# Optimization experiments

Measured on AMD Instinct MI355X. Metric: run time of the kernel, lower is better.

## Reference

```python
import jax, jax.numpy as jnp
import numpy as np

D = 2048
NUM_HEADS = 16
HEAD_DIM = D // NUM_HEADS
B, T = 4, 2048
NEG = -1e9


def setup_inputs() -> dict:
    key = jax.random.key(0)
    ks = jax.random.split(key, 6)
    X = jax.random.normal(ks[0], (B, T, D), dtype=jnp.float32)
    # additive causal mask, broadcast over batch and heads
    causal = jnp.tril(jnp.ones((T, T), dtype=jnp.float32))
    mask = jnp.where(causal == 1, 0.0, NEG)[None, None, :, :]
    scale = np.sqrt(2.0 / D).astype(np.float32)
    wq_w = jax.random.normal(ks[1], (D, D), dtype=jnp.float32) * scale
    wk_w = jax.random.normal(ks[2], (D, D), dtype=jnp.float32) * scale
    wv_w = jax.random.normal(ks[3], (D, D), dtype=jnp.float32) * scale
    wo_w = jax.random.normal(ks[4], (D, D), dtype=jnp.float32) * scale
    zeros = jnp.zeros((D,), dtype=jnp.float32)
    return {
        "X": X, "mask": mask,
        "wq_w": wq_w, "wq_b": zeros,
        "wk_w": wk_w, "wk_b": zeros,
        "wv_w": wv_w, "wv_b": zeros,
        "wo_w": wo_w, "wo_b": zeros,
    }


def reference(X, mask, wq_w, wq_b, wk_w, wk_b, wv_w, wv_b, wo_w, wo_b):
    b, t, d = X.shape
    # project and split heads: [b, h, t, hd]
    def proj(w, bias):
        return (X @ w + bias).reshape(b, t, NUM_HEADS, HEAD_DIM).transpose(0, 2, 1, 3)
    Q = proj(wq_w, wq_b)
    K = proj(wk_w, wk_b)
    V = proj(wv_w, wv_b)
    scores = jnp.einsum("bhqd,bhkd->bhqk", Q, K) / np.sqrt(HEAD_DIM).astype(X.dtype)
    scores = scores + mask
    A = jax.nn.softmax(scores, axis=-1)
    ctx = jnp.einsum("bhqk,bhkd->bhqd", A, V)  # [b, h, t, hd]
    ctx = ctx.transpose(0, 2, 1, 3).reshape(b, t, d)
    return ctx @ wo_w + wo_b
```

## Files before the change

### kernel.cpp

```cpp
#include <hip/hip_runtime.h>
#include <stdint.h>

#define DMODEL 2048
#define NH 16
#define HD 128
#define BATCH 4
#define SEQ 2048
#define MTOT (BATCH * SEQ)
#define LOG2E 1.44269504088896340736f

typedef __bf16 bf16x8 __attribute__((ext_vector_type(8)));
typedef float floatx4 __attribute__((ext_vector_type(4)));

__device__ __forceinline__ uint16_t f2b(float f) {
    union { float f; uint32_t i; } v; v.f = f;
    uint32_t r = v.i + 0x7fffu + ((v.i >> 16) & 1u);
    return (uint16_t)(r >> 16);
}

#define GLD16(gp, lp)                                                          \
    __builtin_amdgcn_global_load_lds(                                          \
        (__attribute__((address_space(1))) unsigned int*)(gp),                 \
        (__attribute__((address_space(3))) unsigned int*)(lp), 16, 0, 0)

#define WAITVMC(N) asm volatile("s_waitcnt vmcnt(" #N ")" ::: "memory")
#define WAITLGKM0                                                              \
    do {                                                                       \
        asm volatile("s_waitcnt lgkmcnt(0)" ::: "memory");                     \
        __builtin_amdgcn_sched_barrier(0);                                     \
    } while (0)

__global__ __launch_bounds__(256) void cvt_bf16(const float* __restrict__ in,
                                                uint16_t* __restrict__ out, int n) {
    const int i = (blockIdx.x * 256 + threadIdx.x) * 8;
    if (i >= n) return;
    const float4 a = *(const float4*)(in + i);
    const float4 b = *(const float4*)(in + i + 4);
    uint16_t v[8] __attribute__((aligned(16))) = {
        f2b(a.x), f2b(a.y), f2b(a.z), f2b(a.w),
        f2b(b.x), f2b(b.y), f2b(b.z), f2b(b.w)};
    *(uint4*)(out + i) = *(const uint4*)v;
}

__global__ __launch_bounds__(256) void tr_wf(const float* __restrict__ in,
                                             uint16_t* __restrict__ out) {
    __shared__ float t[64 * 69];
    const int tid = threadIdx.x;
    const int r0 = blockIdx.y * 64, c0 = blockIdx.x * 64;
    const int rr = tid >> 2, c16 = (tid & 3) << 4;
#pragma unroll
    for (int j = 0; j < 4; j++)
        *(float4*)&t[rr * 69 + c16 + j * 4] =
            *(const float4*)(in + (size_t)(r0 + rr) * DMODEL + c0 + c16 + j * 4);
    __syncthreads();
    const int oc = tid >> 2, r16 = (tid & 3) << 4;
    uint16_t v[16] __attribute__((aligned(16)));
#pragma unroll
    for (int j = 0; j < 16; j++) v[j] = f2b(t[(r16 + j) * 69 + oc]);
    uint16_t* o = out + (size_t)(c0 + oc) * DMODEL + r0 + r16;
    *(uint4*)o = *(const uint4*)v;
    *(uint4*)(o + 8) = *(const uint4*)(v + 8);
}

__global__ __launch_bounds__(512, 2) void gemm256(const uint16_t* __restrict__ A,
                                                  const uint16_t* __restrict__ Bt,
                                                  const float* __restrict__ bias,
                                                  void* __restrict__ Cout,
                                                  float scale, int mode, int tld) {
    __shared__ __attribute__((aligned(16))) uint16_t As[2][32 * 512];
    __shared__ __attribute__((aligned(16))) uint16_t Bs[2][32 * 512];

    const int tid = threadIdx.x, lane = tid & 63, w = tid >> 6;
    const int wr = w >> 2, wc = w & 3;
    const int col = lane & 15, quad = lane >> 4;

    const int nwg = gridDim.x, cpx = nwg >> 3;
    const int swz = ((int)blockIdx.x & 7) * cpx + ((int)blockIdx.x >> 3);
    const long m0 = (long)(swz >> 3) * 256;
    const long n0 = (long)(swz & 7) * 256;

    const uint16_t* Ab = A + (m0 + col) * (size_t)DMODEL + quad * 8;
    const uint16_t* Bb = Bt + (n0 + col) * (size_t)DMODEL + quad * 8;

#define STAGE256(bf, kt)                                                       \
    {                                                                          \
        const size_t kb = (size_t)(kt) * 64;                                   \
        _Pragma("unroll") for (int j = 0; j < 4; j++) {                        \
            const int blk = w * 4 + j;                                         \
            const size_t off =                                                 \
                kb + (size_t)(blk >> 1) * (16 * DMODEL) + (size_t)(blk & 1) * 32; \
            GLD16(Ab + off, &As[bf][blk * 512]);                               \
            GLD16(Bb + off, &Bs[bf][blk * 512]);                               \
        }                                                                      \
    }

    floatx4 acc[8][4];
#pragma unroll
    for (int m = 0; m < 8; m++)
#pragma unroll
        for (int n = 0; n < 4; n++) acc[m][n] = (floatx4){0.f, 0.f, 0.f, 0.f};

    const int NT = DMODEL / 64;
    STAGE256(0, 0);
    STAGE256(1, 1);

#pragma unroll 1
    for (int kt = 0; kt < NT; ++kt) {
        const int cur = kt & 1;
        if (kt == NT - 1) { WAITVMC(0); } else { WAITVMC(8); }
        __builtin_amdgcn_s_barrier();

        bf16x8 a0[8], b0[4];
#pragma unroll
        for (int m = 0; m < 8; m++)
            a0[m] = *(const bf16x8*)&As[cur][((wr * 8 + m) * 2 + 0) * 512 + lane * 8];
#pragma unroll
        for (int n = 0; n < 4; n++)
            b0[n] = *(const bf16x8*)&Bs[cur][((wc * 4 + n) * 2 + 0) * 512 + lane * 8];
        __builtin_amdgcn_s_setprio(1);
#pragma unroll
        for (int m = 0; m < 8; m++)
#pragma unroll
            for (int n = 0; n < 4; n++)
                acc[m][n] = __builtin_amdgcn_mfma_f32_16x16x32_bf16(a0[m], b0[n],
                                                                    acc[m][n], 0, 0, 0);
        __builtin_amdgcn_s_setprio(0);

        bf16x8 a1[8], b1[4];
#pragma unroll
        for (int m = 0; m < 8; m++)
            a1[m] = *(const bf16x8*)&As[cur][((wr * 8 + m) * 2 + 1) * 512 + lane * 8];
#pragma unroll
        for (int n = 0; n < 4; n++)
            b1[n] = *(const bf16x8*)&Bs[cur][((wc * 4 + n) * 2 + 1) * 512 + lane * 8];
        WAITLGKM0;
        __builtin_amdgcn_s_barrier();
        if (kt + 2 < NT) STAGE256(cur, kt + 2);
        __builtin_amdgcn_s_setprio(1);
#pragma unroll
        for (int m = 0; m < 8; m++)
#pragma unroll
            for (int n = 0; n < 4; n++)
                acc[m][n] = __builtin_amdgcn_mfma_f32_16x16x32_bf16(a1[m], b1[n],
                                                                    acc[m][n], 0, 0, 0);
        __builtin_amdgcn_s_setprio(0);
    }

    float bv[4];
#pragma unroll
    for (int n = 0; n < 4; n++) bv[n] = bias[n0 + wc * 64 + n * 16 + col];
#pragma unroll
    for (int m = 0; m < 8; m++) {
        const long row = m0 + wr * 128 + m * 16 + quad * 4;
#pragma unroll
        for (int n = 0; n < 4; n++) {
            const long cc = n0 + wc * 64 + n * 16 + col;
            if (mode == 2) {
                uint16_t tmp[4] __attribute__((aligned(8)));
#pragma unroll
                for (int r = 0; r < 4; r++)
                    tmp[r] = f2b((acc[m][n][r] + bv[n]) * scale);
                *(uint2*)&((uint16_t*)Cout)[(size_t)cc * tld + row] =
                    *(const uint2*)tmp;
            } else {
#pragma unroll
                for (int r = 0; r < 4; r++) {
                    const float v = (acc[m][n][r] + bv[n]) * scale;
                    const long idx = (row + r) * DMODEL + cc;
                    if (mode == 1) ((float*)Cout)[idx] = v;
                    else           ((uint16_t*)Cout)[idx] = f2b(v);
                }
            }
        }
    }
#undef STAGE256
}

__global__ __launch_bounds__(256, 2) void gemm(const uint16_t* __restrict__ A,
                                               const uint16_t* __restrict__ Bt,
                                               const float* __restrict__ bias,
                                               void* __restrict__ Cout,
                                               float scale, int mode, int tld) {
    __shared__ __attribute__((aligned(16))) uint16_t As[128 * 32];
    __shared__ __attribute__((aligned(16))) uint16_t Bs[128 * 32];
    const int tid = threadIdx.x, lane = tid & 63, w = tid >> 6;
    const int wr = w >> 1, wc = w & 1;
    const int col = lane & 15, quad = lane >> 4;
    const long m0 = (long)blockIdx.y * 128, n0 = (long)blockIdx.x * 128;

    floatx4 acc[4][4];
#pragma unroll
    for (int i = 0; i < 4; i++)
#pragma unroll
        for (int j = 0; j < 4; j++) acc[i][j] = (floatx4){0.f, 0.f, 0.f, 0.f};

    const int srow = tid >> 2, sc = (tid & 3) << 3;
    const uint16_t* Ag0 = A + (m0 + srow) * DMODEL + sc;
    const uint16_t* Bg0 = Bt + (n0 + srow) * DMODEL + sc;
    const long rstep = (long)64 * DMODEL;
    uint16_t* AsW = &As[w * 512];
    uint16_t* BsW = &Bs[w * 512];

    for (int kt = 0; kt < DMODEL; kt += 32) {
        GLD16(Ag0 + kt, AsW);
        GLD16(Ag0 + rstep + kt, AsW + 2048);
        GLD16(Bg0 + kt, BsW);
        GLD16(Bg0 + rstep + kt, BsW + 2048);
        __syncthreads();
        bf16x8 af[4], bfr[4];
#pragma unroll
        for (int i = 0; i < 4; i++)
            af[i] = *(const bf16x8*)&As[(wr * 64 + i * 16 + col) * 32 + quad * 8];
#pragma unroll
        for (int j = 0; j < 4; j++)
            bfr[j] = *(const bf16x8*)&Bs[(wc * 64 + j * 16 + col) * 32 + quad * 8];
#pragma unroll
        for (int i = 0; i < 4; i++)
#pragma unroll
            for (int j = 0; j < 4; j++)
                acc[i][j] = __builtin_amdgcn_mfma_f32_16x16x32_bf16(af[i], bfr[j],
                                                                    acc[i][j], 0, 0, 0);
        __syncthreads();
    }

    float bv[4];
#pragma unroll
    for (int j = 0; j < 4; j++) bv[j] = bias[n0 + wc * 64 + j * 16 + col];
#pragma unroll
    for (int i = 0; i < 4; i++) {
        const long row = m0 + wr * 64 + i * 16 + quad * 4;
#pragma unroll
        for (int j = 0; j < 4; j++) {
            const long cc = n0 + wc * 64 + j * 16 + col;
            if (mode == 2) {
                uint16_t tmp[4] __attribute__((aligned(8)));
#pragma unroll
                for (int r = 0; r < 4; r++)
                    tmp[r] = f2b((acc[i][j][r] + bv[j]) * scale);
                *(uint2*)&((uint16_t*)Cout)[(size_t)cc * tld + row] =
                    *(const uint2*)tmp;
            } else {
#pragma unroll
                for (int r = 0; r < 4; r++) {
                    const float v = (acc[i][j][r] + bv[j]) * scale;
                    const long idx = (row + r) * DMODEL + cc;
                    if (mode == 1) ((float*)Cout)[idx] = v;
                    else           ((uint16_t*)Cout)[idx] = f2b(v);
                }
            }
        }
    }
}

__global__ __launch_bounds__(256, 2) void flash(uint16_t* __restrict__ QO,
                                                const uint16_t* __restrict__ Kp,
                                                const uint16_t* __restrict__ Vt,
                                                int vld) {
    __shared__ __attribute__((aligned(16))) uint16_t Ks[16 * 512];
    __shared__ __attribute__((aligned(16))) uint16_t Vs[16 * 512];
    __shared__ __attribute__((aligned(16))) uint16_t Ps[4][32 * 88];

    const int tid = threadIdx.x, lane = tid & 63, w = tid >> 6;
    const int col = lane & 15, quad = lane >> 4;
    const int h = blockIdx.y & 15, b = blockIdx.y >> 4;
    const size_t brow = (size_t)b * SEQ;

    const uint16_t* kbase = Kp + brow * DMODEL + h * HD;
    const uint16_t* vtbase = Vt + (size_t)(h * HD) * vld + brow;
    const uint16_t* kg0 = kbase + (size_t)(w * 16 + col) * DMODEL + quad * 8;
    const uint16_t* vg0 = vtbase + (size_t)(w * 32 + col) * vld + quad * 8;

    for (int half = 0; half < 2; ++half) {
        const int qi = half ? (int)blockIdx.x : (15 - (int)blockIdx.x);
        const int q0 = qi * 128;
        uint16_t* qbase = QO + (brow + q0 + w * 32) * DMODEL + h * HD;

        bf16x8 qf[2][4];
#pragma unroll
        for (int i = 0; i < 2; i++)
#pragma unroll
            for (int kk = 0; kk < 4; kk++)
                qf[i][kk] = *(const bf16x8*)(qbase + (size_t)(i * 16 + col) * DMODEL +
                                             kk * 32 + quad * 8);

        floatx4 accO[2][8];
#pragma unroll
        for (int i = 0; i < 2; i++)
#pragma unroll
            for (int jd = 0; jd < 8; jd++) accO[i][jd] = (floatx4){0.f, 0.f, 0.f, 0.f};
        float mrun[2][4], lrun[2][4];
#pragma unroll
        for (int i = 0; i < 2; i++)
#pragma unroll
            for (int r = 0; r < 4; r++) { mrun[i][r] = -1e30f; lrun[i][r] = 0.f; }

        const int nkt = 2 * qi + 2;

        uint4 kv[4], vv4[4];
        {
#pragma unroll
            for (int p = 0; p < 4; p++)
                kv[p] = *(const uint4*)(kg0 + p * 32);
#pragma unroll
            for (int s = 0; s < 2; s++)
#pragma unroll
                for (int k2 = 0; k2 < 2; k2++)
                    vv4[s * 2 + k2] =
                        *(const uint4*)(vg0 + (size_t)s * 16 * vld + k2 * 32);
        }

        for (int ki = 0; ki < nkt; ki++) {
            const int key0 = ki * 64;
#pragma unroll
            for (int p = 0; p < 4; p++)
                *(uint4*)&Ks[(w * 4 + p) * 512 + lane * 8] = kv[p];
#pragma unroll
            for (int s = 0; s < 2; s++)
#pragma unroll
                for (int k2 = 0; k2 < 2; k2++)
                    *(uint4*)&Vs[((w * 2 + s) * 2 + k2) * 512 + lane * 8] =
                        vv4[s * 2 + k2];
            __syncthreads();

            if (ki + 1 < nkt) {
                const size_t koff = (size_t)(key0 + 64);
#pragma unroll
                for (int p = 0; p < 4; p++)
                    kv[p] = *(const uint4*)(kg0 + koff * DMODEL + p * 32);
#pragma unroll
                for (int s = 0; s < 2; s++)
#pragma unroll
                    for (int k2 = 0; k2 < 2; k2++)
                        vv4[s * 2 + k2] = *(const uint4*)(vg0 + (size_t)s * 16 * vld +
                                                          koff + k2 * 32);
            }

            floatx4 s[2][4];
            __builtin_amdgcn_s_setprio(1);
#pragma unroll
            for (int i = 0; i < 2; i++)
#pragma unroll
                for (int jk = 0; jk < 4; jk++) {
                    floatx4 a = (floatx4){0.f, 0.f, 0.f, 0.f};
#pragma unroll
                    for (int kk = 0; kk < 4; kk++) {
                        bf16x8 bb = *(const bf16x8*)&Ks[(jk * 4 + kk) * 512 + lane * 8];
                        a = __builtin_amdgcn_mfma_f32_16x16x32_bf16(qf[i][kk], bb, a, 0, 0, 0);
                    }
                    s[i][jk] = a;
                }
            __builtin_amdgcn_s_setprio(0);

            if (key0 + 63 > q0 + w * 32) {
#pragma unroll
                for (int i = 0; i < 2; i++) {
                    const int qb = q0 + w * 32 + i * 16 + quad * 4;
#pragma unroll
                    for (int jk = 0; jk < 4; jk++) {
                        const int key = key0 + jk * 16 + col;
#pragma unroll
                        for (int r = 0; r < 4; r++)
                            if (key > qb + r) s[i][jk][r] = -1e30f;
                    }
                }
            }

            float alpha[2][4];
#pragma unroll
            for (int i = 0; i < 2; i++)
#pragma unroll
                for (int r = 0; r < 4; r++) {
                    float mx = s[i][0][r];
#pragma unroll
                    for (int jk = 1; jk < 4; jk++) mx = fmaxf(mx, s[i][jk][r]);
                    mx = fmaxf(mx, __shfl_xor(mx, 1, 64));
                    mx = fmaxf(mx, __shfl_xor(mx, 2, 64));
                    mx = fmaxf(mx, __shfl_xor(mx, 4, 64));
                    mx = fmaxf(mx, __shfl_xor(mx, 8, 64));
                    mx = fmaxf(mx, mrun[i][r]);
                    alpha[i][r] = exp2f((mrun[i][r] - mx) * LOG2E);
                    mrun[i][r] = mx;
                }
#pragma unroll
            for (int i = 0; i < 2; i++)
#pragma unroll
                for (int r = 0; r < 4; r++) {
                    float psum = 0.f;
#pragma unroll
                    for (int jk = 0; jk < 4; jk++) {
                        const float p = exp2f((s[i][jk][r] - mrun[i][r]) * LOG2E);
                        psum += p;
                        Ps[w][(i * 16 + quad * 4 + r) * 88 + jk * 16 + col] = f2b(p);
                    }
                    lrun[i][r] = lrun[i][r] * alpha[i][r] + psum;
                }
#pragma unroll
            for (int i = 0; i < 2; i++)
#pragma unroll
                for (int jd = 0; jd < 8; jd++)
#pragma unroll
                    for (int r = 0; r < 4; r++) accO[i][jd][r] *= alpha[i][r];

            bf16x8 pf[2][2];
#pragma unroll
            for (int i = 0; i < 2; i++)
#pragma unroll
                for (int k2 = 0; k2 < 2; k2++)
                    pf[i][k2] = *(const bf16x8*)&Ps[w][(i * 16 + col) * 88 + k2 * 32 + quad * 8];
            __builtin_amdgcn_s_setprio(1);
#pragma unroll
            for (int jd = 0; jd < 8; jd++)
#pragma unroll
                for (int k2 = 0; k2 < 2; k2++) {
                    bf16x8 vvv = *(const bf16x8*)&Vs[(jd * 2 + k2) * 512 + lane * 8];
#pragma unroll
                    for (int i = 0; i < 2; i++)
                        accO[i][jd] = __builtin_amdgcn_mfma_f32_16x16x32_bf16(pf[i][k2], vvv,
                                                                              accO[i][jd], 0, 0, 0);
                }
            __builtin_amdgcn_s_setprio(0);
            __syncthreads();
        }

        float inv[2][4];
#pragma unroll
        for (int i = 0; i < 2; i++)
#pragma unroll
            for (int r = 0; r < 4; r++) {
                float l = lrun[i][r];
                l += __shfl_xor(l, 1, 64);
                l += __shfl_xor(l, 2, 64);
                l += __shfl_xor(l, 4, 64);
                l += __shfl_xor(l, 8, 64);
                inv[i][r] = 1.0f / l;
            }
#pragma unroll
        for (int i = 0; i < 2; i++)
#pragma unroll
            for (int jd = 0; jd < 8; jd++)
#pragma unroll
                for (int r = 0; r < 4; r++)
                    qbase[(size_t)(i * 16 + quad * 4 + r) * DMODEL + jd * 16 + col] =
                        f2b(accO[i][jd][r] * inv[i][r]);
    }
}

extern "C" void kernel_launch(void* const* d_in, const int* in_sizes, int n_in,
                              void* d_out, int out_size, void* d_ws, size_t ws_size,
                              hipStream_t stream) {
    const float* X   = (const float*)d_in[0];
    float*       msk = (float*)d_in[1];
    const float* wq  = (const float*)d_in[2];
    const float* wqb = (const float*)d_in[3];
    const float* wk  = (const float*)d_in[4];
    const float* wkb = (const float*)d_in[5];
    const float* wv  = (const float*)d_in[6];
    const float* wvb = (const float*)d_in[7];
    const float* wo  = (const float*)d_in[8];
    const float* wob = (const float*)d_in[9];
    float* out = (float*)d_out;

    char* ws = (char*)d_ws;
    const size_t MB = 1ull << 20;
    dim3 tb(256), tb512(512), gT(32, 32);
    const float qs = 0.08838834764831845f;

    if (ws_size >= 136 * MB) {
        uint16_t* Xb = (uint16_t*)(ws);
        uint16_t* Qb = (uint16_t*)(ws + 32 * MB);
        uint16_t* Kb = (uint16_t*)(ws + 64 * MB);
        uint16_t* Vb = (uint16_t*)(ws + 96 * MB);
        uint16_t* Wt = (uint16_t*)(ws + 128 * MB);
        dim3 g256((MTOT / 256) * (DMODEL / 256));
        dim3 gF(8, 64);
        cvt_bf16<<<8192, tb, 0, stream>>>(X, Xb, MTOT * DMODEL);
        tr_wf<<<gT, tb, 0, stream>>>(wq, Wt);
        gemm256<<<g256, tb512, 0, stream>>>(Xb, Wt, wqb, Qb, qs, 0, 0);
        tr_wf<<<gT, tb, 0, stream>>>(wk, Wt);
        gemm256<<<g256, tb512, 0, stream>>>(Xb, Wt, wkb, Kb, 1.0f, 0, 0);
        tr_wf<<<gT, tb, 0, stream>>>(wv, Wt);
        gemm256<<<g256, tb512, 0, stream>>>(Xb, Wt, wvb, Vb, 1.0f, 2, MTOT);
        flash<<<gF, tb, 0, stream>>>(Qb, Kb, Vb, MTOT);
        tr_wf<<<gT, tb, 0, stream>>>(wo, Wt);
        gemm256<<<g256, tb512, 0, stream>>>(Qb, Wt, wob, out, 1.0f, 1, 0);
    } else {
        uint16_t* Xb = (uint16_t*)(ws);
        uint16_t* Qb = (uint16_t*)(ws + 8 * MB);
        uint16_t *Kb, *Vb, *Wt;
        if (ws_size >= 40 * MB) {
            Kb = (uint16_t*)(ws + 16 * MB);
            Vb = (uint16_t*)(ws + 24 * MB);
            Wt = (uint16_t*)(ws + 32 * MB);
        } else {
            Kb = (uint16_t*)msk;
            Vb = Kb + (size_t)SEQ * DMODEL;
            Wt = (uint16_t*)(ws + 16 * MB);
        }
        dim3 gG(16, 16), gF(8, 16);
        for (int b = 0; b < BATCH; b++) {
            const float* Xf = X + (size_t)b * SEQ * DMODEL;
            float* Ob = out + (size_t)b * SEQ * DMODEL;
            cvt_bf16<<<2048, tb, 0, stream>>>(Xf, Xb, SEQ * DMODEL);
            tr_wf<<<gT, tb, 0, stream>>>(wq, Wt);
            gemm<<<gG, tb, 0, stream>>>(Xb, Wt, wqb, Qb, qs, 0, 0);
            tr_wf<<<gT, tb, 0, stream>>>(wk, Wt);
            gemm<<<gG, tb, 0, stream>>>(Xb, Wt, wkb, Kb, 1.0f, 0, 0);
            tr_wf<<<gT, tb, 0, stream>>>(wv, Wt);
            gemm<<<gG, tb, 0, stream>>>(Xb, Wt, wvb, Vb, 1.0f, 2, SEQ);
            flash<<<gF, tb, 0, stream>>>(Qb, Kb, Vb, SEQ);
            tr_wf<<<gT, tb, 0, stream>>>(wo, Wt);
            gemm<<<gG, tb, 0, stream>>>(Qb, Wt, wob, Ob, 1.0f, 1, 0);
        }
    }

    (void)in_sizes; (void)n_in; (void)out_size;
}
```

Baseline: 752.6 us.

## Split 256x256 GEMM main loop into four interleaved load/compute phases

Restructures the large-tile GEMM k-loop into four phases, each reading half the A fragments and staging a quarter of the next tiles' global-to-LDS loads between barriers. The aim is to interleave memory staging with MFMA work at finer granularity and to cut register pressure by holding 4 A fragments instead of 8. In exchange it adds more barriers per iteration and needs more delicate vmcnt bookkeeping, which risks added sync stalls or subtle ordering errors.

Measured after the change: 714.2 us. 5.1% less time.

```diff
diff --git a/kernel.cpp b/kernel.cpp
--- a/kernel.cpp
+++ b/kernel.cpp
@@ -81,70 +81,75 @@
 
     const uint16_t* Ab = A + (m0 + col) * (size_t)DMODEL + quad * 8;
     const uint16_t* Bb = Bt + (n0 + col) * (size_t)DMODEL + quad * 8;
-
-#define STAGE256(bf, kt)                                                       \
-    {                                                                          \
-        const size_t kb = (size_t)(kt) * 64;                                   \
-        _Pragma("unroll") for (int j = 0; j < 4; j++) {                        \
-            const int blk = w * 4 + j;                                         \
-            const size_t off =                                                 \
-                kb + (size_t)(blk >> 1) * (16 * DMODEL) + (size_t)(blk & 1) * 32; \
-            GLD16(Ab + off, &As[bf][blk * 512]);                               \
-            GLD16(Bb + off, &Bs[bf][blk * 512]);                               \
+    const int g0 = w * 2, g1 = w * 2 + 1;
+
+#define STG_A(bf, kt, kk)                                                      \
+    do {                                                                       \
+        GLD16(Ab + (size_t)(g0 * 16) * DMODEL + (kt) * 64 + (kk) * 32,         \
+              &As[bf][(g0 * 2 + (kk)) * 512]);                                 \
+        GLD16(Ab + (size_t)(g1 * 16) * DMODEL + (kt) * 64 + (kk) * 32,         \
+              &As[bf][(g1 * 2 + (kk)) * 512]);                                 \
+    } while (0)
+#define STG_B(bf, kt, kk)                                                      \
+    do {                                                                       \
+        GLD16(Bb + (size_t)(g0 * 16) * DMODEL + (kt) * 64 + (kk) * 32,         \
+              &Bs[bf][(g0 * 2 + (kk)) * 512]);                                 \
+        GLD16(Bb + (size_t)(g1 * 16) * DMODEL + (kt) * 64 + (kk) * 32,         \
+              &Bs[bf][(g1 * 2 + (kk)) * 512]);                                 \
+    } while (0)
+
+    floatx4 acc[8][4];
+#pragma unroll
+    for (int m = 0; m < 8; m++)
+#pragma unroll
+        for (int n = 0; n < 4; n++) acc[m][n] = (floatx4){0.f, 0.f, 0.f, 0.f};
+
+    const int NT = DMODEL / 64;
+    STG_A(0, 0, 0); STG_B(0, 0, 0);
+    STG_A(0, 0, 1); STG_B(0, 0, 1);
+    STG_A(1, 1, 0); STG_B(1, 1, 0);
+    WAITVMC(8);
+    __builtin_amdgcn_s_barrier();
+
+    bf16x8 afr[4], bfr[4];
+
+#define PHASE(MS, KK, READB, STAGE_STMT, TAILW)                                \
+    do {                                                                       \
+        if (READB) {                                                           \
+            _Pragma("unroll") for (int n = 0; n < 4; n++)                      \
+                bfr[n] = *(const bf16x8*)&Bs[cur][((wc * 4 + n) * 2 + (KK)) *  \
+                                                     512 + lane * 8];          \
         }                                                                      \
+        _Pragma("unroll") for (int m = 0; m < 4; m++)                          \
+            afr[m] = *(const bf16x8*)&As[cur][((wr * 8 + (MS)*4 + m) * 2 +     \
+                                               (KK)) * 512 + lane * 8];        \
+        STAGE_STMT;                                                            \
+        __builtin_amdgcn_s_barrier();                                          \
+        WAITLGKM0;                                                             \
+        __builtin_amdgcn_s_setprio(1);                                         \
+        _Pragma("unroll") for (int m = 0; m < 4; m++)                          \
+            _Pragma("unroll") for (int n = 0; n < 4; n++)                      \
+                acc[(MS)*4 + m][n] = __builtin_amdgcn_mfma_f32_16x16x32_bf16(  \
+                    afr[m], bfr[n], acc[(MS)*4 + m][n], 0, 0, 0);              \
+        __builtin_amdgcn_s_setprio(0);                                         \
+        TAILW;                                                                 \
+        __builtin_amdgcn_s_barrier();                                          \
+    } while (0)
+
+#pragma unroll 1
+    for (int t = 0; t < NT; ++t) {
+        const int cur = t & 1, nxt = cur ^ 1;
+        PHASE(0, 0, 1, { if (t + 1 < NT) STG_A(nxt, t + 1, 1); }, {});
+        PHASE(1, 0, 0, { if (t + 1 < NT) STG_B(nxt, t + 1, 1); },
+              { if (t == NT - 1) { WAITVMC(0); } else { WAITVMC(8); } });
+        PHASE(0, 1, 1, { if (t + 2 < NT) STG_A(cur, t + 2, 0); }, {});
+        PHASE(1, 1, 0, { if (t + 2 < NT) STG_B(cur, t + 2, 0); },
+              { if (t == NT - 2) { WAITVMC(2); }
+                else if (t < NT - 2) { WAITVMC(8); } });
     }
-
-    floatx4 acc[8][4];
-#pragma unroll
-    for (int m = 0; m < 8; m++)
-#pragma unroll
-        for (int n = 0; n < 4; n++) acc[m][n] = (floatx4){0.f, 0.f, 0.f, 0.f};
-
-    const int NT = DMODEL / 64;
-    STAGE256(0, 0);
-    STAGE256(1, 1);
-
-#pragma unroll 1
-    for (int kt = 0; kt < NT; ++kt) {
-        const int cur = kt & 1;
-        if (kt == NT - 1) { WAITVMC(0); } else { WAITVMC(8); }
-        __builtin_amdgcn_s_barrier();
-
-        bf16x8 a0[8], b0[4];
-#pragma unroll
-        for (int m = 0; m < 8; m++)
-            a0[m] = *(const bf16x8*)&As[cur][((wr * 8 + m) * 2 + 0) * 512 + lane * 8];
-#pragma unroll
-        for (int n = 0; n < 4; n++)
-            b0[n] = *(const bf16x8*)&Bs[cur][((wc * 4 + n) * 2 + 0) * 512 + lane * 8];
-        __builtin_amdgcn_s_setprio(1);
-#pragma unroll
-        for (int m = 0; m < 8; m++)
-#pragma unroll
-            for (int n = 0; n < 4; n++)
-                acc[m][n] = __builtin_amdgcn_mfma_f32_16x16x32_bf16(a0[m], b0[n],
-                                                                    acc[m][n], 0, 0, 0);
-        __builtin_amdgcn_s_setprio(0);
-
-        bf16x8 a1[8], b1[4];
-#pragma unroll
-        for (int m = 0; m < 8; m++)
-            a1[m] = *(const bf16x8*)&As[cur][((wr * 8 + m) * 2 + 1) * 512 + lane * 8];
-#pragma unroll
-        for (int n = 0; n < 4; n++)
-            b1[n] = *(const bf16x8*)&Bs[cur][((wc * 4 + n) * 2 + 1) * 512 + lane * 8];
-        WAITLGKM0;
-        __builtin_amdgcn_s_barrier();
-        if (kt + 2 < NT) STAGE256(cur, kt + 2);
-        __builtin_amdgcn_s_setprio(1);
-#pragma unroll
-        for (int m = 0; m < 8; m++)
-#pragma unroll
-            for (int n = 0; n < 4; n++)
-                acc[m][n] = __builtin_amdgcn_mfma_f32_16x16x32_bf16(a1[m], b1[n],
-                                                                    acc[m][n], 0, 0, 0);
-        __builtin_amdgcn_s_setprio(0);
-    }
+#undef PHASE
+#undef STG_A
+#undef STG_B
 
     float bv[4];
 #pragma unroll
@@ -173,7 +178,6 @@
             }
         }
     }
-#undef STAGE256
 }
 
 __global__ __launch_bounds__(256, 2) void gemm(const uint16_t* __restrict__ A,
```
